# Performance work log

Measured on AMD Instinct MI355X. Metric: run time of the kernel, lower is better.

## Reference

```python
import jax, jax.numpy as jnp
import numpy as np

ALPHA = 0.2          # LeakyReLU negative slope
NEG_INF = -9e15      # masking value from the original module


def setup_inputs() -> dict:
    key = jax.random.key(0)
    kw, ka, k1, k2, k3 = jax.random.split(key, 5)
    B, N1, N2, F, O = 4, 2048, 2048, 256, 256
    word = jax.random.normal(kw, (B, N2, F), dtype=jnp.float32)
    # 0/1 hypergraph incidence matrix (float, as in the torch module)
    adj = jax.random.randint(ka, (B, N1, N2), 0, 2).astype(jnp.float32)
    stdv = 1.0 / np.sqrt(O)
    W1 = jax.random.uniform(k1, (F, O), jnp.float32, -stdv, stdv)
    W2 = jax.random.uniform(k2, (F, O), jnp.float32, -stdv, stdv)
    w3 = jax.random.uniform(k3, (2 * O, 1), jnp.float32, -stdv, stdv)
    return {"word": word, "adj": adj, "W1": W1, "W2": W2, "w3": w3}


def reference(word, adj, W1, W2, w3):
    # word: [B, N2, F]; adj: [B, N1, N2]; W1/W2: [F, O]; w3: [2O, 1]
    O = W1.shape[1]
    # mean-pool neighbor features per hyperedge (row-normalized adj)
    deg = jnp.sum(adj, axis=-1, keepdims=True)                 # [B, N1, 1]
    deg = jnp.where(deg > 0, deg, jnp.ones_like(deg))
    mp = jnp.matmul(adj / deg, word)                           # [B, N1, F]
    # The original builds 4D tensors h1[b,i,j,:] = adj[b,i,j]*word[b,j,:] and
    # h_mp[b,i,j,:] = adj[b,i,j]*mp[b,i,:], projects both and dots with w3.
    # Since scaling commutes with the linear maps, the scalar score is
    #   adj[b,i,j] * (word[b,j] @ W1 @ w3_a + mp[b,i] @ W2 @ w3_b)
    w3a = w3[:O, 0]                                            # pairs with w1h
    w3b = w3[O:, 0]                                            # pairs with w2h
    s1 = jnp.einsum('bnf,fo,o->bn', word, W1, w3a)             # [B, N2]
    s2 = jnp.einsum('bnf,fo,o->bn', mp, W2, w3b)               # [B, N1]
    pre = adj * (s2[:, :, None] + s1[:, None, :])              # [B, N1, N2]
    alpha = jnp.exp(jax.nn.leaky_relu(pre, ALPHA))
    attention = jnp.where(adj > 0, alpha, NEG_INF)
    attention_edge = jax.nn.softmax(attention, axis=2)         # over N2
    edge = jnp.matmul(attention_edge, word)                    # [B, N1, F]
    return edge
```

## Files before the change

kernel.cpp:

```cpp
#include <hip/hip_runtime.h>

#define B 4
#define N 2048
#define F 256
#define O 256
#define LOG2E 1.4426950408889634f
#define NEG_BIG -9000000000000000.0f

typedef _Float16 f16;
typedef f16 f16x8 __attribute__((ext_vector_type(8)));
typedef f16 f16x4 __attribute__((ext_vector_type(4)));
typedef float f32x4 __attribute__((ext_vector_type(4)));

#define WS_V1 0
#define WS_V2 256
#define WS_T1 512
#define WS_T2 (512 + B*N)
#define WS_S2 (512 + 2*B*N)
#define WS_CR (512 + 3*B*N)
#define WS_WN (512 + 4*B*N)
#define WT_OFF (1u << 20)
#define MK_OFF (6u << 20)

__device__ __forceinline__ float alpha_of(float pre2) {
  return __builtin_amdgcn_exp2f(fmaxf(pre2, 0.2f * pre2));
}

__global__ __launch_bounds__(256) void k_v(const float* __restrict__ W1,
                                           const float* __restrict__ W2,
                                           const float* __restrict__ w3,
                                           float* __restrict__ ws) {
  int tid = threadIdx.x;
  int lane = tid & 63;
  int f = blockIdx.x * 4 + (tid >> 6);
  float a = 0.f, b = 0.f;
  #pragma unroll
  for (int k = 0; k < 4; ++k) {
    int o = lane + 64 * k;
    a += W1[f * O + o] * w3[o];
    b += W2[f * O + o] * w3[O + o];
  }
  #pragma unroll
  for (int off = 32; off > 0; off >>= 1) {
    a += __shfl_down(a, off);
    b += __shfl_down(b, off);
  }
  if (lane == 0) {
    ws[WS_V1 + f] = a;
    ws[WS_V2 + f] = b;
  }
}

__global__ __launch_bounds__(256) void k_t(const float* __restrict__ word,
                                           float* __restrict__ ws) {
  const float* v1 = ws + WS_V1;
  const float* v2 = ws + WS_V2;
  int row = blockIdx.x;
  int f = threadIdx.x;
  float w = word[(size_t)row * F + f];
  float a = w * v1[f];
  float b = w * v2[f];
  #pragma unroll
  for (int off = 32; off > 0; off >>= 1) {
    a += __shfl_down(a, off);
    b += __shfl_down(b, off);
  }
  __shared__ float sa[4], sb[4];
  int wid = f >> 6;
  if ((f & 63) == 0) { sa[wid] = a; sb[wid] = b; }
  __syncthreads();
  if (f == 0) {
    ws[WS_T1 + row] = (sa[0] + sa[1] + sa[2] + sa[3]) * LOG2E;
    ws[WS_T2 + row] = sb[0] + sb[1] + sb[2] + sb[3];
  }
}

__global__ __launch_bounds__(256) void k_tr(const float* __restrict__ word,
                                            f16* __restrict__ wordT) {
  __shared__ float tile[64][65];
  int t = threadIdx.x;
  int k0 = blockIdx.x * 64, f0 = blockIdx.y * 64, b = blockIdx.z;
  #pragma unroll
  for (int it = 0; it < 4; ++it) {
    int r = (t >> 4) + it * 16;
    int c = (t & 15) * 4;
    float4 v = *(const float4*)(word + ((size_t)b * N + k0 + r) * F + f0 + c);
    tile[r][c] = v.x; tile[r][c + 1] = v.y; tile[r][c + 2] = v.z; tile[r][c + 3] = v.w;
  }
  __syncthreads();
  #pragma unroll
  for (int it = 0; it < 2; ++it) {
    int fr = (t >> 3) + it * 32;
    int kc = (t & 7) * 8;
    f16x8 h;
    #pragma unroll
    for (int j = 0; j < 8; ++j) h[j] = (f16)tile[kc + j][fr];
    *(f16x8*)(wordT + ((size_t)(b * F + f0 + fr)) * N + k0 + kc) = h;
  }
}

__global__ __launch_bounds__(256) void k_stats(const float* __restrict__ adj,
                                               float* __restrict__ ws,
                                               unsigned char* __restrict__ mask) {
  int row = blockIdx.x;
  int b = row >> 11;
  int t = threadIdx.x;
  int wid = t >> 6, lane = t & 63;
  const float* arow = adj + (size_t)row * N;
  const float* t1b = ws + WS_T1 + b * N;
  const float* t2b = ws + WS_T2 + b * N;

  float4 a0 = *(const float4*)(arow + t * 8);
  float4 a1 = *(const float4*)(arow + t * 8 + 4);
  float4 u0 = *(const float4*)(t2b + t * 8);
  float4 u1 = *(const float4*)(t2b + t * 8 + 4);
  float deg = a0.x + a0.y + a0.z + a0.w + a1.x + a1.y + a1.z + a1.w;
  float dot = a0.x * u0.x + a0.y * u0.y + a0.z * u0.z + a0.w * u0.w +
              a1.x * u1.x + a1.y * u1.y + a1.z * u1.z + a1.w * u1.w;
  unsigned mb = (a0.x > 0.f ? 1u : 0u) | (a0.y > 0.f ? 2u : 0u) |
                (a0.z > 0.f ? 4u : 0u) | (a0.w > 0.f ? 8u : 0u) |
                (a1.x > 0.f ? 16u : 0u) | (a1.y > 0.f ? 32u : 0u) |
                (a1.z > 0.f ? 64u : 0u) | (a1.w > 0.f ? 128u : 0u);
  mask[(size_t)row * 256 + t] = (unsigned char)mb;

  #pragma unroll
  for (int off = 32; off > 0; off >>= 1) {
    deg += __shfl_down(deg, off);
    dot += __shfl_down(dot, off);
  }
  __shared__ float rd[4], rt[4], rm[4], rz[4];
  if (lane == 0) { rd[wid] = deg; rt[wid] = dot; }
  __syncthreads();
  deg = rd[0] + rd[1] + rd[2] + rd[3];
  dot = rt[0] + rt[1] + rt[2] + rt[3];
  float degc = deg > 0.f ? deg : 1.f;
  float s2p = (dot / degc) * LOG2E;

  float4 p0 = *(const float4*)(t1b + t * 8);
  float4 p1 = *(const float4*)(t1b + t * 8 + 4);
  float al[8];
  al[0] = (mb & 1)   ? alpha_of(p0.x + s2p) : NEG_BIG;
  al[1] = (mb & 2)   ? alpha_of(p0.y + s2p) : NEG_BIG;
  al[2] = (mb & 4)   ? alpha_of(p0.z + s2p) : NEG_BIG;
  al[3] = (mb & 8)   ? alpha_of(p0.w + s2p) : NEG_BIG;
  al[4] = (mb & 16)  ? alpha_of(p1.x + s2p) : NEG_BIG;
  al[5] = (mb & 32)  ? alpha_of(p1.y + s2p) : NEG_BIG;
  al[6] = (mb & 64)  ? alpha_of(p1.z + s2p) : NEG_BIG;
  al[7] = (mb & 128) ? alpha_of(p1.w + s2p) : NEG_BIG;
  float m = NEG_BIG;
  #pragma unroll
  for (int j = 0; j < 8; ++j) m = fmaxf(m, al[j]);
  #pragma unroll
  for (int off = 32; off > 0; off >>= 1) m = fmaxf(m, __shfl_down(m, off));
  if (lane == 0) rm[wid] = m;
  __syncthreads();
  m = fmaxf(fmaxf(rm[0], rm[1]), fmaxf(rm[2], rm[3]));

  float negmL = -m * LOG2E;
  float z = 0.f;
  #pragma unroll
  for (int j = 0; j < 8; ++j) z += __builtin_amdgcn_exp2f(fmaf(al[j], LOG2E, negmL));
  #pragma unroll
  for (int off = 32; off > 0; off >>= 1) z += __shfl_down(z, off);
  if (lane == 0) rz[wid] = z;
  __syncthreads();
  if (t == 0) {
    z = rz[0] + rz[1] + rz[2] + rz[3];
    ws[WS_S2 + row] = s2p;
    if (deg > 0.f) {
      ws[WS_CR + row] = negmL - log2f(z);
      ws[WS_WN + row] = 0.f;
    } else {
      ws[WS_CR + row] = 0.f;
      ws[WS_WN + row] = 1.0f / (float)N;
    }
  }
}

#define TR 32
#define TF 128
#define BK 32
#define AP 40

__global__ __launch_bounds__(256) void k_gemm(const f16* __restrict__ wordT,
                                              const unsigned char* __restrict__ maskg,
                                              const float* __restrict__ ws,
                                              float* __restrict__ out) {
  __shared__ __align__(16) f16 Bs[TF][AP];
  __shared__ __align__(16) f16 Aw[TR][AP];
  __shared__ __align__(16) float t1S[N];
  __shared__ __align__(16) unsigned maskS[TR][64];
  __shared__ float sS2[TR], sCR[TR], sWN[TR];

  int t = threadIdx.x;
  int rb = blockIdx.x >> 1, fh = blockIdx.x & 1;
  int row0 = rb * TR, fblk = fh * TF;
  int b = row0 >> 11;

  {
    const float* t1g = ws + WS_T1 + b * N;
    *(float4*)(t1S + t * 8)     = *(const float4*)(t1g + t * 8);
    *(float4*)(t1S + t * 8 + 4) = *(const float4*)(t1g + t * 8 + 4);
    const uint4* mg = (const uint4*)(maskg + (size_t)(row0 + (t >> 3)) * 256 + (t & 7) * 32);
    uint4* md = (uint4*)&maskS[t >> 3][(t & 7) * 8];
    md[0] = mg[0]; md[1] = mg[1];
    if (t < TR) {
      sS2[t] = ws[WS_S2 + row0 + t];
      sCR[t] = ws[WS_CR + row0 + t];
      sWN[t] = ws[WS_WN + row0 + t];
    }
  }
  __syncthreads();

  int wr = t >> 3, wg = t & 7;
  float rs2 = sS2[wr], rcr = sCR[wr], rwn = sWN[wr];

  int wid = t >> 6, l = t & 63;
  int h = wid & 1, q2 = wid >> 1;
  int q = l >> 4, li = l & 15;

  f32x4 acc[4] = {{0,0,0,0},{0,0,0,0},{0,0,0,0},{0,0,0,0}};

  const f16* bsrc = wordT + ((size_t)(b * F + fblk + (t >> 1))) * N + (t & 1) * 16;

  for (int k0 = 0; k0 < N; k0 += BK) {
    {
      const uint4* src = (const uint4*)(bsrc + k0);
      uint4 v0 = src[0], v1 = src[1];
      uint4* dst = (uint4*)&Bs[t >> 1][(t & 1) * 16];
      dst[0] = v0; dst[1] = v1;
    }
    {
      unsigned mw = maskS[wr][k0 >> 5];
      float4 tv = *(const float4*)(t1S + k0 + wg * 4);
      float wv[4];
      const float tvv[4] = {tv.x, tv.y, tv.z, tv.w};
      #pragma unroll
      for (int j = 0; j < 4; ++j) {
        float al = alpha_of(tvv[j] + rs2);
        float wsel = __builtin_amdgcn_exp2f(fmaf(al, LOG2E, rcr));
        wv[j] = ((mw >> (wg * 4 + j)) & 1) ? wsel : rwn;
      }
      f16x4 hw;
      #pragma unroll
      for (int j = 0; j < 4; ++j) hw[j] = (f16)wv[j];
      *(f16x4*)(&Aw[wr][wg * 4]) = hw;
    }
    __syncthreads();

    const f16x8 af = *(const f16x8*)(&Aw[h * 16 + li][q * 8]);
    #pragma unroll
    for (int ft = 0; ft < 4; ++ft) {
      const f16x8 bf = *(const f16x8*)(&Bs[q2 * 64 + ft * 16 + li][q * 8]);
      acc[ft] = __builtin_amdgcn_mfma_f32_16x16x32_f16(af, bf, acc[ft], 0, 0, 0);
    }
    __syncthreads();
  }

  #pragma unroll
  for (int ft = 0; ft < 4; ++ft) {
    int gf = fblk + q2 * 64 + ft * 16 + li;
    #pragma unroll
    for (int i = 0; i < 4; ++i) {
      int gr = row0 + h * 16 + q * 4 + i;
      out[(size_t)gr * F + gf] = acc[ft][i];
    }
  }
}

extern "C" void kernel_launch(void* const* d_in, const int* in_sizes, int n_in,
                              void* d_out, int out_size, void* d_ws, size_t ws_size,
                              hipStream_t stream) {
  const float* word = (const float*)d_in[0];
  const float* adj  = (const float*)d_in[1];
  const float* W1   = (const float*)d_in[2];
  const float* W2   = (const float*)d_in[3];
  const float* w3   = (const float*)d_in[4];
  float* out = (float*)d_out;
  float* ws  = (float*)d_ws;
  f16* wordT = (f16*)((char*)d_ws + WT_OFF);
  unsigned char* mask = (unsigned char*)d_ws + MK_OFF;

  k_v<<<64, 256, 0, stream>>>(W1, W2, w3, ws);
  k_t<<<B * N, 256, 0, stream>>>(word, ws);
  k_tr<<<dim3(N / 64, F / 64, B), 256, 0, stream>>>(word, wordT);
  k_stats<<<B * N, 256, 0, stream>>>(adj, ws, mask);
  k_gemm<<<(B * N / TR) * (F / TF), 256, 0, stream>>>(wordT, mask, ws, out);
}
```

Baseline: 154.4 us.

## Fuse score and transpose prep kernels; restructure GEMM with 32x32 MFMA and double buffering

The two kernels that computed per-row scores and built the fp16 transposed word matrix become one kernel, so word is read once instead of twice. The GEMM is rewritten so each 512-thread block covers all 256 output features for 32 rows. It uses 32x32x16 MFMA, loads B fragments straight from global memory into registers with no LDS staging, and double-buffers the generated attention-weight tile. This stops the attention weights being generated twice, once per feature half, and cuts the number of barriers, at the cost of more register pressure and uncoalesced-looking direct global B loads.

```diff
diff --git a/kernel.cpp b/kernel.cpp
--- a/kernel.cpp
+++ b/kernel.cpp
@@ -10,7 +10,7 @@
 typedef _Float16 f16;
 typedef f16 f16x8 __attribute__((ext_vector_type(8)));
 typedef f16 f16x4 __attribute__((ext_vector_type(4)));
-typedef float f32x4 __attribute__((ext_vector_type(4)));
+typedef float f32x16 __attribute__((ext_vector_type(16)));
 
 #define WS_V1 0
 #define WS_V2 256
@@ -51,52 +51,52 @@
   }
 }
 
-__global__ __launch_bounds__(256) void k_t(const float* __restrict__ word,
-                                           float* __restrict__ ws) {
-  const float* v1 = ws + WS_V1;
-  const float* v2 = ws + WS_V2;
-  int row = blockIdx.x;
-  int f = threadIdx.x;
-  float w = word[(size_t)row * F + f];
-  float a = w * v1[f];
-  float b = w * v2[f];
-  #pragma unroll
-  for (int off = 32; off > 0; off >>= 1) {
-    a += __shfl_down(a, off);
-    b += __shfl_down(b, off);
-  }
-  __shared__ float sa[4], sb[4];
-  int wid = f >> 6;
-  if ((f & 63) == 0) { sa[wid] = a; sb[wid] = b; }
-  __syncthreads();
-  if (f == 0) {
-    ws[WS_T1 + row] = (sa[0] + sa[1] + sa[2] + sa[3]) * LOG2E;
-    ws[WS_T2 + row] = sb[0] + sb[1] + sb[2] + sb[3];
-  }
-}
-
-__global__ __launch_bounds__(256) void k_tr(const float* __restrict__ word,
-                                            f16* __restrict__ wordT) {
-  __shared__ float tile[64][65];
+__global__ __launch_bounds__(256) void k_prep(const float* __restrict__ word,
+                                              float* __restrict__ ws,
+                                              f16* __restrict__ wordT) {
+  __shared__ float v1s[F], v2s[F];
+  __shared__ __align__(16) f16 tile[F][40];
   int t = threadIdx.x;
-  int k0 = blockIdx.x * 64, f0 = blockIdx.y * 64, b = blockIdx.z;
-  #pragma unroll
-  for (int it = 0; it < 4; ++it) {
-    int r = (t >> 4) + it * 16;
-    int c = (t & 15) * 4;
-    float4 v = *(const float4*)(word + ((size_t)b * N + k0 + r) * F + f0 + c);
-    tile[r][c] = v.x; tile[r][c + 1] = v.y; tile[r][c + 2] = v.z; tile[r][c + 3] = v.w;
-  }
-  __syncthreads();
-  #pragma unroll
-  for (int it = 0; it < 2; ++it) {
-    int fr = (t >> 3) + it * 32;
-    int kc = (t & 7) * 8;
-    f16x8 h;
-    #pragma unroll
-    for (int j = 0; j < 8; ++j) h[j] = (f16)tile[kc + j][fr];
-    *(f16x8*)(wordT + ((size_t)(b * F + f0 + fr)) * N + k0 + kc) = h;
-  }
+  int k0 = blockIdx.x * 32;
+  int b = blockIdx.y;
+
+  if (t < 64)       ((float4*)v1s)[t]      = ((const float4*)(ws + WS_V1))[t];
+  else if (t < 128) ((float4*)v2s)[t - 64] = ((const float4*)(ws + WS_V2))[t - 64];
+  __syncthreads();
+
+  int r = t >> 3;
+  int cg = t & 7;
+  const float* wrow = word + ((size_t)(b * N + k0 + r)) * F;
+  float a = 0.f, bb = 0.f;
+  #pragma unroll
+  for (int i = 0; i < 8; ++i) {
+    int c = i * 32 + cg * 4;
+    float4 w = *(const float4*)(wrow + c);
+    float4 x1 = *(const float4*)(v1s + c);
+    float4 x2 = *(const float4*)(v2s + c);
+    a  += w.x * x1.x + w.y * x1.y + w.z * x1.z + w.w * x1.w;
+    bb += w.x * x2.x + w.y * x2.y + w.z * x2.z + w.w * x2.w;
+    tile[c + 0][r] = (f16)w.x;
+    tile[c + 1][r] = (f16)w.y;
+    tile[c + 2][r] = (f16)w.z;
+    tile[c + 3][r] = (f16)w.w;
+  }
+  #pragma unroll
+  for (int off = 4; off > 0; off >>= 1) {
+    a  += __shfl_down(a, off);
+    bb += __shfl_down(bb, off);
+  }
+  if (cg == 0) {
+    ws[WS_T1 + b * N + k0 + r] = a * LOG2E;
+    ws[WS_T2 + b * N + k0 + r] = bb;
+  }
+  __syncthreads();
+
+  f16* dst = wordT + ((size_t)(b * F + t)) * N + k0;
+  *(f16x8*)(dst + 0)  = *(const f16x8*)&tile[t][0];
+  *(f16x8*)(dst + 8)  = *(const f16x8*)&tile[t][8];
+  *(f16x8*)(dst + 16) = *(const f16x8*)&tile[t][16];
+  *(f16x8*)(dst + 24) = *(const f16x8*)&tile[t][24];
 }
 
 __global__ __launch_bounds__(256) void k_stats(const float* __restrict__ adj,
@@ -177,94 +177,84 @@
   }
 }
 
-#define TR 32
-#define TF 128
-#define BK 32
-#define AP 40
-
-__global__ __launch_bounds__(256) void k_gemm(const f16* __restrict__ wordT,
-                                              const unsigned char* __restrict__ maskg,
-                                              const float* __restrict__ ws,
-                                              float* __restrict__ out) {
-  __shared__ __align__(16) f16 Bs[TF][AP];
-  __shared__ __align__(16) f16 Aw[TR][AP];
+__global__ __launch_bounds__(512, 2) void k_gemm(const f16* __restrict__ wordT,
+                                                 const unsigned char* __restrict__ maskg,
+                                                 const float* __restrict__ ws,
+                                                 float* __restrict__ out) {
+  __shared__ __align__(16) f16 Aw[2][8][512];
   __shared__ __align__(16) float t1S[N];
-  __shared__ __align__(16) unsigned maskS[TR][64];
-  __shared__ float sS2[TR], sCR[TR], sWN[TR];
-
-  int t = threadIdx.x;
-  int rb = blockIdx.x >> 1, fh = blockIdx.x & 1;
-  int row0 = rb * TR, fblk = fh * TF;
-  int b = row0 >> 11;
-
-  {
-    const float* t1g = ws + WS_T1 + b * N;
-    *(float4*)(t1S + t * 8)     = *(const float4*)(t1g + t * 8);
-    *(float4*)(t1S + t * 8 + 4) = *(const float4*)(t1g + t * 8 + 4);
-    const uint4* mg = (const uint4*)(maskg + (size_t)(row0 + (t >> 3)) * 256 + (t & 7) * 32);
-    uint4* md = (uint4*)&maskS[t >> 3][(t & 7) * 8];
-    md[0] = mg[0]; md[1] = mg[1];
-    if (t < TR) {
-      sS2[t] = ws[WS_S2 + row0 + t];
-      sCR[t] = ws[WS_CR + row0 + t];
-      sWN[t] = ws[WS_WN + row0 + t];
+  __shared__ __align__(16) unsigned maskS[32][64];
+  __shared__ float sSC[96];
+
+  const int t = threadIdx.x;
+  const int row0 = blockIdx.x * 32;
+  const int b = row0 >> 11;
+
+  *(float4*)&t1S[t * 4] = *(const float4*)(ws + WS_T1 + b * N + t * 4);
+  *(uint4*)&maskS[t >> 4][(t & 15) * 4] =
+      *(const uint4*)(maskg + (size_t)(row0 + (t >> 4)) * 256 + (t & 15) * 16);
+  if (t < 32) {
+    sSC[t]      = ws[WS_S2 + row0 + t];
+    sSC[32 + t] = ws[WS_CR + row0 + t];
+    sSC[64 + t] = ws[WS_WN + row0 + t];
+  }
+  __syncthreads();
+
+  const int gl = t & 63;
+  const int gc = t >> 6;
+  const int grow = gl & 31;
+  const int gkb = gc * 16 + (gl >> 5) * 8;
+  const float rs2 = sSC[grow], rcr = sSC[32 + grow], rwn = sSC[64 + grow];
+
+  const int lw = t & 63;
+  const int wv = t >> 6;
+  const int fcol = wv * 32 + (lw & 31);
+  const f16* bptr = wordT + ((size_t)(b * F + fcol)) * N + (lw >> 5) * 8;
+
+  f32x16 acc = {0.f,0.f,0.f,0.f,0.f,0.f,0.f,0.f,0.f,0.f,0.f,0.f,0.f,0.f,0.f,0.f};
+
+  #define GENW(IT, BUF)                                                        \
+    {                                                                          \
+      const int kg = (IT) * 128 + gkb;                                         \
+      const unsigned mw = maskS[grow][kg >> 5] >> (kg & 31);                   \
+      const float4 tv0 = *(const float4*)&t1S[kg];                             \
+      const float4 tv1 = *(const float4*)&t1S[kg + 4];                         \
+      const float tvv[8] = {tv0.x, tv0.y, tv0.z, tv0.w,                        \
+                            tv1.x, tv1.y, tv1.z, tv1.w};                       \
+      f16x8 h;                                                                 \
+      _Pragma("unroll")                                                        \
+      for (int j = 0; j < 8; ++j) {                                            \
+        float p = tvv[j] + rs2;                                                \
+        float al = __builtin_amdgcn_exp2f(fmaxf(p, 0.2f * p));                 \
+        float wsel = __builtin_amdgcn_exp2f(fmaf(al, LOG2E, rcr));             \
+        float w = ((mw >> j) & 1u) ? wsel : rwn;                               \
+        h[j] = (f16)w;                                                         \
+      }                                                                        \
+      *(f16x8*)&Aw[BUF][gc][gl * 8] = h;                                       \
     }
-  }
-  __syncthreads();
-
-  int wr = t >> 3, wg = t & 7;
-  float rs2 = sS2[wr], rcr = sCR[wr], rwn = sWN[wr];
-
-  int wid = t >> 6, l = t & 63;
-  int h = wid & 1, q2 = wid >> 1;
-  int q = l >> 4, li = l & 15;
-
-  f32x4 acc[4] = {{0,0,0,0},{0,0,0,0},{0,0,0,0},{0,0,0,0}};
-
-  const f16* bsrc = wordT + ((size_t)(b * F + fblk + (t >> 1))) * N + (t & 1) * 16;
-
-  for (int k0 = 0; k0 < N; k0 += BK) {
-    {
-      const uint4* src = (const uint4*)(bsrc + k0);
-      uint4 v0 = src[0], v1 = src[1];
-      uint4* dst = (uint4*)&Bs[t >> 1][(t & 1) * 16];
-      dst[0] = v0; dst[1] = v1;
-    }
-    {
-      unsigned mw = maskS[wr][k0 >> 5];
-      float4 tv = *(const float4*)(t1S + k0 + wg * 4);
-      float wv[4];
-      const float tvv[4] = {tv.x, tv.y, tv.z, tv.w};
-      #pragma unroll
-      for (int j = 0; j < 4; ++j) {
-        float al = alpha_of(tvv[j] + rs2);
-        float wsel = __builtin_amdgcn_exp2f(fmaf(al, LOG2E, rcr));
-        wv[j] = ((mw >> (wg * 4 + j)) & 1) ? wsel : rwn;
-      }
-      f16x4 hw;
-      #pragma unroll
-      for (int j = 0; j < 4; ++j) hw[j] = (f16)wv[j];
-      *(f16x4*)(&Aw[wr][wg * 4]) = hw;
+
+  GENW(0, 0)
+  __syncthreads();
+
+  for (int it = 0; it < 16; ++it) {
+    const int cur = it & 1;
+    f16x8 bf[8];
+    const f16* bp = bptr + it * 128;
+    #pragma unroll
+    for (int c = 0; c < 8; ++c) bf[c] = *(const f16x8*)(bp + c * 16);
+    if (it < 15) GENW(it + 1, cur ^ 1)
+    #pragma unroll
+    for (int c = 0; c < 8; ++c) {
+      const f16x8 af = *(const f16x8*)&Aw[cur][c][lw * 8];
+      acc = __builtin_amdgcn_mfma_f32_32x32x16_f16(af, bf[c], acc, 0, 0, 0);
     }
     __syncthreads();
-
-    const f16x8 af = *(const f16x8*)(&Aw[h * 16 + li][q * 8]);
-    #pragma unroll
-    for (int ft = 0; ft < 4; ++ft) {
-      const f16x8 bf = *(const f16x8*)(&Bs[q2 * 64 + ft * 16 + li][q * 8]);
-      acc[ft] = __builtin_amdgcn_mfma_f32_16x16x32_f16(af, bf, acc[ft], 0, 0, 0);
-    }
-    __syncthreads();
-  }
-
-  #pragma unroll
-  for (int ft = 0; ft < 4; ++ft) {
-    int gf = fblk + q2 * 64 + ft * 16 + li;
-    #pragma unroll
-    for (int i = 0; i < 4; ++i) {
-      int gr = row0 + h * 16 + q * 4 + i;
-      out[(size_t)gr * F + gf] = acc[ft][i];
-    }
+  }
+
+  #pragma unroll
+  for (int reg = 0; reg < 16; ++reg) {
+    int lr = (reg & 3) + 8 * (reg >> 2) + 4 * (lw >> 5);
+    out[(size_t)(row0 + lr) * F + fcol] = acc[reg];
   }
 }
 
@@ -282,8 +272,7 @@
   unsigned char* mask = (unsigned char*)d_ws + MK_OFF;
 
   k_v<<<64, 256, 0, stream>>>(W1, W2, w3, ws);
-  k_t<<<B * N, 256, 0, stream>>>(word, ws);
-  k_tr<<<dim3(N / 64, F / 64, B), 256, 0, stream>>>(word, wordT);
+  k_prep<<<dim3(N / 32, B), 256, 0, stream>>>(word, ws, wordT);
   k_stats<<<B * N, 256, 0, stream>>>(adj, ws, mask);
-  k_gemm<<<(B * N / TR) * (F / TF), 256, 0, stream>>>(wordT, mask, ws, out);
-}
+  k_gemm<<<(B * N) / 32, 512, 0, stream>>>(wordT, mask, ws, out);
+}
```

Measured after the change: 148.5 us. -3.8%, faster.
